# Kernel optimization log

Measured on AMD Instinct MI355X. Metric: run time of the kernel, lower is better.

## Reference

```python
import jax, jax.numpy as jnp
import numpy as np

SHIFT, REDUCE = 1, 2  # PAD = 0


def setup_inputs() -> dict:
    key = jax.random.key(0)
    k1, k2, k3 = jax.random.split(key, 3)
    B, L, E, H = 64, 128, 1024, 1024
    sentence = jax.random.normal(k1, (B, L, E), dtype=jnp.float32)
    T = 2 * L - 1
    # Valid left-branching transition sequence: S, S, R, S, R, S, R, ...
    tr = np.ones(T, dtype=np.int64)
    tr[2::2] = REDUCE
    transitions = jnp.asarray(np.tile(tr, (B, 1)))
    # word projection: Linear(E -> 2H); reduce (TreeLSTM) cell: Linear(2H -> 5H)
    Ww = (jax.random.normal(k2, (E, 2 * H), dtype=jnp.float32) * 0.02)
    bw = jnp.zeros((2 * H,), dtype=jnp.float32)
    Wr = (jax.random.normal(k3, (2 * H, 5 * H), dtype=jnp.float32) * 0.02)
    br = jnp.zeros((5 * H,), dtype=jnp.float32)
    return {"sentence": sentence, "transitions": transitions,
            "Ww": Ww, "bw": bw, "Wr": Wr, "br": br}


def _spinn_fwd(sentence, transitions, Ww, bw, Wr, br):
    B, L, _ = sentence.shape
    H = Ww.shape[1] // 2
    # word projection, split into (h, c) halves (batch norm / dropout disabled)
    out = sentence @ Ww + bw                      # [B, L, 2H]
    h_buf, c_buf = jnp.split(out, 2, axis=2)      # each [B, L, H]
    S = L + 1                                     # thin-stack capacity (+1 scratch)
    bidx = jnp.arange(B)

    def step(carry, act):
        sh, sc, sp, bp = carry                    # stacks [B,S,H], ptrs [B]
        is_shift = act == SHIFT
        is_red = act == REDUCE
        # buffer front word (front-to-back pop)
        bp_c = jnp.clip(bp, 0, L - 1)
        buf_h = h_buf[bidx, bp_c]
        buf_c = c_buf[bidx, bp_c]
        # stack top two: right = top, left = second
        ri = jnp.clip(sp - 1, 0, S - 1)
        li = jnp.clip(sp - 2, 0, S - 1)
        rh, rc = sh[bidx, ri], sc[bidx, ri]
        lh, lc = sh[bidx, li], sc[bidx, li]
        # TreeLSTM reduce cell
        a = jnp.concatenate([lh, rh], axis=-1) @ Wr + br   # [B, 5H]
        i, fl, fr, o, g = jnp.split(a, 5, axis=-1)
        c_new = (jax.nn.sigmoid(fl) * lc + jax.nn.sigmoid(fr) * rc
                 + jax.nn.sigmoid(i) * jnp.tanh(g))
        h_new = jax.nn.sigmoid(o) * jnp.tanh(c_new)
        # select write value/index; PAD writes to index S which is dropped
        wh = jnp.where(is_shift[:, None], buf_h, h_new)
        wc = jnp.where(is_shift[:, None], buf_c, c_new)
        widx = jnp.where(is_shift, sp, jnp.where(is_red, sp - 2, S))
        sh = sh.at[bidx, widx].set(wh, mode='drop')
        sc = sc.at[bidx, widx].set(wc, mode='drop')
        sp = sp + jnp.where(is_shift, 1, jnp.where(is_red, -1, 0))
        bp = bp + is_shift.astype(bp.dtype)
        return (sh, sc, sp, bp), None

    init = (jnp.zeros((B, S, H), sentence.dtype),
            jnp.zeros((B, S, H), sentence.dtype),
            jnp.zeros((B,), jnp.int32),
            jnp.zeros((B,), jnp.int32))
    acts = transitions.T.astype(jnp.int32)        # [T, B], time-major
    (sh, sc, sp, bp), _ = jax.lax.scan(step, init, acts)
    # final stack has size 1; peek h
    return sh[bidx, jnp.clip(sp - 1, 0, S - 1)]   # [B, H]


def reference(sentence, transitions, Ww, bw, Wr, br):
    return _spinn_fwd(sentence, transitions, Ww, bw, Wr, br)
```

## Files before the change

kernel.cpp:

```cpp
#include <hip/hip_runtime.h>

typedef float  f4v __attribute__((ext_vector_type(4)));
typedef short  s8v __attribute__((ext_vector_type(8)));

#define B_   64
#define L_   128
#define T_   255
#define RMAX 127
#define BPK_HALF 5242880

__device__ __forceinline__ unsigned short f2bf(float f) {
    union { float f; unsigned int u; } v; v.f = f;
    unsigned int u = v.u;
    unsigned int r = u + 0x7fffu + ((u >> 16) & 1u);
    return (unsigned short)(r >> 16);
}
__device__ __forceinline__ float bf2f(unsigned short s) {
    union { unsigned int u; float f; } v; v.u = ((unsigned int)s) << 16;
    return v.f;
}
__device__ __forceinline__ float sigf(float x) { return 1.f / (1.f + expf(-x)); }

__global__ void k_transpose_bf16(const float* __restrict__ in, unsigned short* __restrict__ out, int K, int N) {
    __shared__ float tile[32][33];
    int n0 = blockIdx.x * 32, k0 = blockIdx.y * 32;
    int tx = threadIdx.x, ty = threadIdx.y;
    for (int i = ty; i < 32; i += 8) tile[i][tx] = in[(size_t)(k0 + i) * N + n0 + tx];
    __syncthreads();
    for (int i = ty; i < 32; i += 8) out[(size_t)(n0 + i) * K + k0 + tx] = f2bf(tile[tx][i]);
}

__global__ void k_pack_b(const unsigned short* __restrict__ wrt, unsigned short* __restrict__ bpk) {
    int u = blockIdx.x * 256 + threadIdx.x;
    int half = u / 655360;
    int v = u % 655360;
    int cg = v / 10240;
    int rem = v % 10240;
    int g = rem / 2048;
    int rem2 = rem % 2048;
    int kk = rem2 >> 6, lane = rem2 & 63;
    int col = g * 1024 + cg * 16 + (lane & 15);
    int kb = kk * 32 + (lane >> 4) * 8;
    s8v val = *(const s8v*)(wrt + (size_t)col * 2048 + half * 1024 + kb);
    *(s8v*)(bpk + (size_t)u * 8) = val;
}

__global__ void k_control(const int* __restrict__ tr, int* __restrict__ desc) {
    if (threadIdx.x != 0 || blockIdx.x != 0) return;
    int stack[140];
    int sp = 0, bp = 0, r = 0;
    for (int t = 0; t < T_; ++t) {
        int a = tr[t];
        if (a == 1) {
            if (bp < L_) { stack[sp++] = bp; bp++; }
        } else if (a == 2) {
            if (sp >= 2) {
                int right = stack[sp - 1], left = stack[sp - 2];
                sp -= 2;
                desc[2 + r] = left;
                desc[2 + RMAX + r] = right;
                stack[sp++] = -(r + 1);
                r++;
            }
        }
    }
    desc[0] = r;
    desc[1] = (sp > 0) ? stack[sp - 1] : 0;
}

__global__ __launch_bounds__(256) void k_proj2(const float* __restrict__ sentence,
                                               const unsigned short* __restrict__ wwt,
                                               const float* __restrict__ bw,
                                               unsigned short* __restrict__ hw,
                                               float* __restrict__ cw) {
    __shared__ unsigned short lA[128 * 64];
    __shared__ unsigned short lB[128 * 64];
    int tid = threadIdx.x, wv = tid >> 6, lane = tid & 63;
    int lr = lane & 15, lq = lane >> 4;
    int wr = wv >> 1, wc = wv & 1;
    int rb = blockIdx.y * 128, cb = blockIdx.x * 128;
    f4v acc[4][4];
    #pragma unroll
    for (int i = 0; i < 4; ++i)
        #pragma unroll
        for (int j = 0; j < 4; ++j) acc[i][j] = (f4v){0.f, 0.f, 0.f, 0.f};

    for (int ks = 0; ks < 1024; ks += 64) {
        #pragma unroll
        for (int t = 0; t < 4; ++t) {
            int p = t * 256 + tid;
            int row = p >> 3, kgs = p & 7, kg = kgs ^ (row & 7);
            const float* s8 = sentence + (size_t)(rb + row) * 1024 + ks + kg * 8;
            float4 v0 = *(const float4*)(s8);
            float4 v1 = *(const float4*)(s8 + 4);
            s8v av;
            av[0] = (short)f2bf(v0.x); av[1] = (short)f2bf(v0.y);
            av[2] = (short)f2bf(v0.z); av[3] = (short)f2bf(v0.w);
            av[4] = (short)f2bf(v1.x); av[5] = (short)f2bf(v1.y);
            av[6] = (short)f2bf(v1.z); av[7] = (short)f2bf(v1.w);
            *(s8v*)(lA + (size_t)p * 8) = av;
            *(s8v*)(lB + (size_t)p * 8) = *(const s8v*)(wwt + (size_t)(cb + row) * 1024 + ks + kg * 8);
        }
        __syncthreads();
        #pragma unroll
        for (int s = 0; s < 2; ++s) {
            int kgx = (s * 4 + lq) ^ (lr & 7);
            s8v a[4], b[4];
            #pragma unroll
            for (int i = 0; i < 4; ++i) {
                int rowa = wr * 64 + i * 16 + lr;
                int rowb = wc * 64 + i * 16 + lr;
                a[i] = *(const s8v*)(lA + (size_t)(rowa * 8 + kgx) * 8);
                b[i] = *(const s8v*)(lB + (size_t)(rowb * 8 + kgx) * 8);
            }
            #pragma unroll
            for (int i = 0; i < 4; ++i)
                #pragma unroll
                for (int j = 0; j < 4; ++j)
                    acc[i][j] = __builtin_amdgcn_mfma_f32_16x16x32_bf16(a[i], b[j], acc[i][j], 0, 0, 0);
        }
        __syncthreads();
    }
    bool isH = (cb < 1024);
    #pragma unroll
    for (int j = 0; j < 4; ++j) {
        int col = cb + wc * 64 + j * 16 + lr;
        float bias = bw[col];
        #pragma unroll
        for (int i = 0; i < 4; ++i) {
            #pragma unroll
            for (int jj = 0; jj < 4; ++jj) {
                int m = rb + wr * 64 + i * 16 + lq * 4 + jj;
                float v = acc[i][j][jj] + bias;
                if (isH) hw[(size_t)m * 1024 + col] = f2bf(v);
                else     cw[(size_t)m * 1024 + (col - 1024)] = v;
            }
        }
    }
}

__global__ __launch_bounds__(256) void k_pw(const int* __restrict__ desc,
                                            const unsigned short* __restrict__ hw,
                                            const unsigned short* __restrict__ wrt,
                                            const float* __restrict__ br,
                                            unsigned short* __restrict__ pwb) {
    __shared__ unsigned short lA[128 * 64];
    __shared__ unsigned short lB[128 * 64];
    int tid = threadIdx.x, wv = tid >> 6, lane = tid & 63;
    int lr = lane & 15, lq = lane >> 4;
    int wr = wv >> 1, wc = wv & 1;
    int cb = blockIdx.x * 128;
    int r0 = blockIdx.y * 2;
    int nred = desc[0];
    int s0[2], s1[2];
    s0[0] = (r0 < nred) ? desc[2 + r0] : -1;
    s0[1] = (r0 < nred) ? desc[2 + RMAX + r0] : -1;
    s1[0] = (r0 + 1 < nred) ? desc[2 + r0 + 1] : -1;
    s1[1] = (r0 + 1 < nred) ? desc[2 + RMAX + r0 + 1] : -1;
    bool need[2];
    need[0] = (s0[0] >= 0) || (s1[0] >= 0);
    need[1] = (s0[1] >= 0) || (s1[1] >= 0);

    int clist[32], ncl = 0;
    if (need[0]) {
        for (int c = 0; c < 16; ++c) clist[ncl++] = c;
    }
    if (need[1]) {
        for (int c = 16; c < 32; ++c) clist[ncl++] = c;
    }

    f4v acc[4][4];
    #pragma unroll
    for (int i = 0; i < 4; ++i)
        #pragma unroll
        for (int j = 0; j < 4; ++j) acc[i][j] = (f4v){0.f, 0.f, 0.f, 0.f};

    s8v ra[4], rb_[4];
    auto preload = [&](int c) {
        int side = c >> 4;
        int kloc = (c & 15) * 64;
        #pragma unroll
        for (int t = 0; t < 4; ++t) {
            int p = t * 256 + tid;
            int row = p >> 3, kgs = p & 7, kg = kgs ^ (row & 7);
            int m = row & 63;
            int src = (row >> 6) ? s1[side] : s0[side];
            s8v va = (s8v){0,0,0,0,0,0,0,0};
            if (src >= 0)
                va = *(const s8v*)(hw + (size_t)(m * L_ + src) * 1024 + kloc + kg * 8);
            ra[t] = va;
            rb_[t] = *(const s8v*)(wrt + (size_t)(cb + row) * 2048 + side * 1024 + kloc + kg * 8);
        }
    };

    if (ncl > 0) preload(clist[0]);
    for (int ci = 0; ci < ncl; ++ci) {
        #pragma unroll
        for (int t = 0; t < 4; ++t) {
            int p = t * 256 + tid;
            *(s8v*)(lA + (size_t)p * 8) = ra[t];
            *(s8v*)(lB + (size_t)p * 8) = rb_[t];
        }
        __syncthreads();
        if (ci + 1 < ncl) preload(clist[ci + 1]);
        #pragma unroll
        for (int s = 0; s < 2; ++s) {
            int kgx = (s * 4 + lq) ^ (lr & 7);
            s8v a[4], b[4];
            #pragma unroll
            for (int i = 0; i < 4; ++i) {
                int rowa = wr * 64 + i * 16 + lr;
                int rowb = wc * 64 + i * 16 + lr;
                a[i] = *(const s8v*)(lA + (size_t)(rowa * 8 + kgx) * 8);
                b[i] = *(const s8v*)(lB + (size_t)(rowb * 8 + kgx) * 8);
            }
            #pragma unroll
            for (int i = 0; i < 4; ++i)
                #pragma unroll
                for (int j = 0; j < 4; ++j)
                    acc[i][j] = __builtin_amdgcn_mfma_f32_16x16x32_bf16(a[i], b[j], acc[i][j], 0, 0, 0);
        }
        __syncthreads();
    }
    #pragma unroll
    for (int j = 0; j < 4; ++j) {
        int col = cb + wc * 64 + j * 16 + lr;
        float bias = br[col];
        #pragma unroll
        for (int i = 0; i < 4; ++i) {
            #pragma unroll
            for (int jj = 0; jj < 4; ++jj) {
                int prow = wr * 64 + i * 16 + lq * 4 + jj;
                int rr = r0 + (prow >> 6), m = prow & 63;
                if (rr < nred)
                    pwb[((size_t)rr * B_ + m) * 5120 + col] = f2bf(acc[i][j][jj] + bias);
            }
        }
    }
}

__global__ __launch_bounds__(256) void k_step(const int* __restrict__ desc,
                                              const float* __restrict__ cw,
                                              const unsigned short* __restrict__ bpk,
                                              const unsigned short* __restrict__ pwb,
                                              unsigned short* __restrict__ hpk,
                                              unsigned short* __restrict__ nhb,
                                              float* __restrict__ nc,
                                              int r) {
    int nred = desc[0];
    if (r >= nred) return;
    int ls = desc[2 + r], rs = desc[2 + RMAX + r];
    __shared__ float scr[4 * 5 * 16 * 17];
    int tid = threadIdx.x, kq = tid >> 6, lane = tid & 63;
    int bid = blockIdx.x;
    int cg = (bid & 7) * 8 + ((bid >> 3) & 7);
    int rh = bid >> 6;
    int lr = lane & 15, lq = lane >> 4;

    int m_e = tid >> 4, ci_e = tid & 15;
    int mg_e = rh * 16 + m_e, chh_e = cg * 16 + ci_e;
    float pw_pre[5];
    #pragma unroll
    for (int g = 0; g < 5; ++g)
        pw_pre[g] = bf2f(pwb[((size_t)r * B_ + mg_e) * 5120 + g * 1024 + chh_e]);
    float lc = (ls >= 0) ? cw[(size_t)(mg_e * L_ + ls) * 1024 + chh_e]
                         : nc[((size_t)(-1 - ls) * B_ + mg_e) * 1024 + chh_e];
    float rc = (rs >= 0) ? cw[(size_t)(mg_e * L_ + rs) * 1024 + chh_e]
                         : nc[((size_t)(-1 - rs) * B_ + mg_e) * 1024 + chh_e];

    f4v acc[5];
    #pragma unroll
    for (int g = 0; g < 5; ++g) acc[g] = (f4v){0.f, 0.f, 0.f, 0.f};

    #pragma unroll
    for (int side = 0; side < 2; ++side) {
        int src = side ? rs : ls;
        if (src >= 0) continue;
        const unsigned short* A = hpk + (size_t)(-1 - src) * 65536;
        const unsigned short* Bb = bpk + (size_t)side * BPK_HALF;
        #pragma unroll
        for (int kki = 0; kki < 8; ++kki) {
            int kk = kq * 8 + kki;
            s8v a = *(const s8v*)(A + (size_t)((rh * 32 + kk) * 64 + lane) * 8);
            #pragma unroll
            for (int g = 0; g < 5; ++g) {
                s8v b = *(const s8v*)(Bb + (size_t)((((size_t)cg * 5 + g) * 32 + kk) * 64 + lane) * 8);
                acc[g] = __builtin_amdgcn_mfma_f32_16x16x32_bf16(a, b, acc[g], 0, 0, 0);
            }
        }
    }
    #pragma unroll
    for (int g = 0; g < 5; ++g)
        #pragma unroll
        for (int jj = 0; jj < 4; ++jj)
            scr[((kq * 5 + g) * 16 + lq * 4 + jj) * 17 + lr] = acc[g][jj];
    __syncthreads();
    float gg[5];
    #pragma unroll
    for (int g = 0; g < 5; ++g) {
        float s = pw_pre[g];
        #pragma unroll
        for (int q = 0; q < 4; ++q) s += scr[((q * 5 + g) * 16 + m_e) * 17 + ci_e];
        gg[g] = s;
    }
    float cn = sigf(gg[1]) * lc + sigf(gg[2]) * rc + sigf(gg[0]) * tanhf(gg[4]);
    float hn = sigf(gg[3]) * tanhf(cn);
    unsigned short hb = f2bf(hn);
    nc[((size_t)r * B_ + mg_e) * 1024 + chh_e] = cn;
    nhb[((size_t)r * B_ + mg_e) * 1024 + chh_e] = hb;
    int rf = mg_e >> 4, lr2 = mg_e & 15, kk2 = chh_e >> 5, lq2 = (chh_e >> 3) & 3, j = chh_e & 7;
    hpk[(size_t)r * 65536 + (size_t)((rf * 32 + kk2) * 64 + lq2 * 16 + lr2) * 8 + j] = hb;
}

__global__ void k_final(const int* __restrict__ desc,
                        const unsigned short* __restrict__ hw,
                        const unsigned short* __restrict__ nhb,
                        float* __restrict__ out) {
    int idx = blockIdx.x * 256 + threadIdx.x;
    if (idx >= B_ * 1024) return;
    int m = idx >> 10, ch = idx & 1023;
    int fs = desc[1];
    const unsigned short* src = (fs >= 0)
        ? hw  + ((size_t)(m * L_ + fs) << 10) + ch
        : nhb + ((size_t)((-1 - fs) * B_ + m) << 10) + ch;
    out[idx] = bf2f(*src);
}

extern "C" void kernel_launch(void* const* d_in, const int* in_sizes, int n_in,
                              void* d_out, int out_size, void* d_ws, size_t ws_size,
                              hipStream_t stream) {
    const float* sentence = (const float*)d_in[0];
    const int*   trans    = (const int*)d_in[1];
    const float* Ww       = (const float*)d_in[2];
    const float* bw       = (const float*)d_in[3];
    const float* Wr       = (const float*)d_in[4];
    const float* br       = (const float*)d_in[5];
    float* out = (float*)d_out;

    char* w = (char*)d_ws;
    size_t off = 0;
    unsigned short* Wrt = (unsigned short*)(w + off); off += (size_t)5120 * 2048 * 2;
    unsigned short* Wwt = (unsigned short*)(w + off); off += (size_t)2048 * 1024 * 2;
    unsigned short* bpk = (unsigned short*)(w + off); off += (size_t)2 * BPK_HALF * 2;
    unsigned short* hw  = (unsigned short*)(w + off); off += (size_t)8192 * 1024 * 2;
    float*          cw  = (float*)(w + off);          off += (size_t)8192 * 1024 * 4;
    unsigned short* nhb = (unsigned short*)(w + off); off += (size_t)RMAX * B_ * 1024 * 2;
    float*          nc  = (float*)(w + off);          off += (size_t)RMAX * B_ * 1024 * 4;
    unsigned short* hpk = (unsigned short*)(w + off); off += (size_t)RMAX * 65536 * 2;
    unsigned short* pwb = (unsigned short*)(w + off); off += (size_t)RMAX * B_ * 5120 * 2;
    int*            desc = (int*)(w + off);           off += 1024;

    k_transpose_bf16<<<dim3(2048 / 32, 1024 / 32), dim3(32, 8), 0, stream>>>(Ww, Wwt, 1024, 2048);
    k_transpose_bf16<<<dim3(5120 / 32, 2048 / 32), dim3(32, 8), 0, stream>>>(Wr, Wrt, 2048, 5120);
    k_pack_b<<<dim3(5120), dim3(256), 0, stream>>>(Wrt, bpk);
    k_control<<<dim3(1), dim3(1), 0, stream>>>(trans, desc);
    k_proj2<<<dim3(16, 64), dim3(256), 0, stream>>>(sentence, Wwt, bw, hw, cw);
    k_pw<<<dim3(40, 64), dim3(256), 0, stream>>>(desc, hw, Wrt, br, pwb);
    for (int r = 0; r < RMAX; ++r)
        k_step<<<dim3(256), dim3(256), 0, stream>>>(desc, cw, bpk, pwb, hpk, nhb, nc, r);
    k_final<<<dim3((B_ * 1024 + 255) / 256), dim3(256), 0, stream>>>(desc, hw, nhb, out);
}
```

Measured before the change: 1.093 ms.

## Split step K-loop over 8 waves, remap pw blocks per XCD, use nontemporal stores

```diff
diff --git a/kernel.cpp b/kernel.cpp
--- a/kernel.cpp
+++ b/kernel.cpp
@@ -133,7 +133,7 @@
                 int m = rb + wr * 64 + i * 16 + lq * 4 + jj;
                 float v = acc[i][j][jj] + bias;
                 if (isH) hw[(size_t)m * 1024 + col] = f2bf(v);
-                else     cw[(size_t)m * 1024 + (col - 1024)] = v;
+                else     __builtin_nontemporal_store(v, &cw[(size_t)m * 1024 + (col - 1024)]);
             }
         }
     }
@@ -149,8 +149,13 @@
     int tid = threadIdx.x, wv = tid >> 6, lane = tid & 63;
     int lr = lane & 15, lq = lane >> 4;
     int wr = wv >> 1, wc = wv & 1;
-    int cb = blockIdx.x * 128;
-    int r0 = blockIdx.y * 2;
+    int bid = blockIdx.x;
+    int xcd = bid & 7;
+    int s = bid >> 3;
+    int ct = xcd * 5 + (s % 5);
+    int rp = s / 5;
+    int cb = ct * 128;
+    int r0 = rp * 2;
     int nred = desc[0];
     int s0[2], s1[2];
     s0[0] = (r0 < nred) ? desc[2 + r0] : -1;
@@ -204,8 +209,8 @@
         __syncthreads();
         if (ci + 1 < ncl) preload(clist[ci + 1]);
         #pragma unroll
-        for (int s = 0; s < 2; ++s) {
-            int kgx = (s * 4 + lq) ^ (lr & 7);
+        for (int s2 = 0; s2 < 2; ++s2) {
+            int kgx = (s2 * 4 + lq) ^ (lr & 7);
             s8v a[4], b[4];
             #pragma unroll
             for (int i = 0; i < 4; ++i) {
@@ -232,14 +237,16 @@
             for (int jj = 0; jj < 4; ++jj) {
                 int prow = wr * 64 + i * 16 + lq * 4 + jj;
                 int rr = r0 + (prow >> 6), m = prow & 63;
-                if (rr < nred)
-                    pwb[((size_t)rr * B_ + m) * 5120 + col] = f2bf(acc[i][j][jj] + bias);
-            }
-        }
-    }
-}
-
-__global__ __launch_bounds__(256) void k_step(const int* __restrict__ desc,
+                if (rr < nred) {
+                    unsigned short ov = f2bf(acc[i][j][jj] + bias);
+                    __builtin_nontemporal_store(ov, &pwb[((size_t)rr * B_ + m) * 5120 + col]);
+                }
+            }
+        }
+    }
+}
+
+__global__ __launch_bounds__(512) void k_step(const int* __restrict__ desc,
                                               const float* __restrict__ cw,
                                               const unsigned short* __restrict__ bpk,
                                               const unsigned short* __restrict__ pwb,
@@ -250,23 +257,26 @@
     int nred = desc[0];
     if (r >= nred) return;
     int ls = desc[2 + r], rs = desc[2 + RMAX + r];
-    __shared__ float scr[4 * 5 * 16 * 17];
+    __shared__ float scr[8 * 5 * 16 * 17];
     int tid = threadIdx.x, kq = tid >> 6, lane = tid & 63;
     int bid = blockIdx.x;
     int cg = (bid & 7) * 8 + ((bid >> 3) & 7);
     int rh = bid >> 6;
     int lr = lane & 15, lq = lane >> 4;
 
-    int m_e = tid >> 4, ci_e = tid & 15;
+    int m_e = (tid & 255) >> 4, ci_e = tid & 15;
     int mg_e = rh * 16 + m_e, chh_e = cg * 16 + ci_e;
-    float pw_pre[5];
-    #pragma unroll
-    for (int g = 0; g < 5; ++g)
-        pw_pre[g] = bf2f(pwb[((size_t)r * B_ + mg_e) * 5120 + g * 1024 + chh_e]);
-    float lc = (ls >= 0) ? cw[(size_t)(mg_e * L_ + ls) * 1024 + chh_e]
-                         : nc[((size_t)(-1 - ls) * B_ + mg_e) * 1024 + chh_e];
-    float rc = (rs >= 0) ? cw[(size_t)(mg_e * L_ + rs) * 1024 + chh_e]
-                         : nc[((size_t)(-1 - rs) * B_ + mg_e) * 1024 + chh_e];
+    float pw_pre[5] = {0.f, 0.f, 0.f, 0.f, 0.f};
+    float lc = 0.f, rc = 0.f;
+    if (tid < 256) {
+        #pragma unroll
+        for (int g = 0; g < 5; ++g)
+            pw_pre[g] = bf2f(__builtin_nontemporal_load(&pwb[((size_t)r * B_ + mg_e) * 5120 + g * 1024 + chh_e]));
+        lc = (ls >= 0) ? __builtin_nontemporal_load(&cw[(size_t)(mg_e * L_ + ls) * 1024 + chh_e])
+                       : __builtin_nontemporal_load(&nc[((size_t)(-1 - ls) * B_ + mg_e) * 1024 + chh_e]);
+        rc = (rs >= 0) ? __builtin_nontemporal_load(&cw[(size_t)(mg_e * L_ + rs) * 1024 + chh_e])
+                       : __builtin_nontemporal_load(&nc[((size_t)(-1 - rs) * B_ + mg_e) * 1024 + chh_e]);
+    }
 
     f4v acc[5];
     #pragma unroll
@@ -279,8 +289,8 @@
         const unsigned short* A = hpk + (size_t)(-1 - src) * 65536;
         const unsigned short* Bb = bpk + (size_t)side * BPK_HALF;
         #pragma unroll
-        for (int kki = 0; kki < 8; ++kki) {
-            int kk = kq * 8 + kki;
+        for (int kki = 0; kki < 4; ++kki) {
+            int kk = kq * 4 + kki;
             s8v a = *(const s8v*)(A + (size_t)((rh * 32 + kk) * 64 + lane) * 8);
             #pragma unroll
             for (int g = 0; g < 5; ++g) {
@@ -295,21 +305,23 @@
         for (int jj = 0; jj < 4; ++jj)
             scr[((kq * 5 + g) * 16 + lq * 4 + jj) * 17 + lr] = acc[g][jj];
     __syncthreads();
-    float gg[5];
-    #pragma unroll
-    for (int g = 0; g < 5; ++g) {
-        float s = pw_pre[g];
-        #pragma unroll
-        for (int q = 0; q < 4; ++q) s += scr[((q * 5 + g) * 16 + m_e) * 17 + ci_e];
-        gg[g] = s;
-    }
-    float cn = sigf(gg[1]) * lc + sigf(gg[2]) * rc + sigf(gg[0]) * tanhf(gg[4]);
-    float hn = sigf(gg[3]) * tanhf(cn);
-    unsigned short hb = f2bf(hn);
-    nc[((size_t)r * B_ + mg_e) * 1024 + chh_e] = cn;
-    nhb[((size_t)r * B_ + mg_e) * 1024 + chh_e] = hb;
-    int rf = mg_e >> 4, lr2 = mg_e & 15, kk2 = chh_e >> 5, lq2 = (chh_e >> 3) & 3, j = chh_e & 7;
-    hpk[(size_t)r * 65536 + (size_t)((rf * 32 + kk2) * 64 + lq2 * 16 + lr2) * 8 + j] = hb;
+    if (tid < 256) {
+        float gg[5];
+        #pragma unroll
+        for (int g = 0; g < 5; ++g) {
+            float s = pw_pre[g];
+            #pragma unroll
+            for (int q = 0; q < 8; ++q) s += scr[((q * 5 + g) * 16 + m_e) * 17 + ci_e];
+            gg[g] = s;
+        }
+        float cn = sigf(gg[1]) * lc + sigf(gg[2]) * rc + sigf(gg[0]) * tanhf(gg[4]);
+        float hn = sigf(gg[3]) * tanhf(cn);
+        unsigned short hb = f2bf(hn);
+        __builtin_nontemporal_store(cn, &nc[((size_t)r * B_ + mg_e) * 1024 + chh_e]);
+        __builtin_nontemporal_store(hb, &nhb[((size_t)r * B_ + mg_e) * 1024 + chh_e]);
+        int rf = mg_e >> 4, lr2 = mg_e & 15, kk2 = chh_e >> 5, lq2 = (chh_e >> 3) & 3, j = chh_e & 7;
+        __builtin_nontemporal_store(hb, &hpk[(size_t)r * 65536 + (size_t)((rf * 32 + kk2) * 64 + lq2 * 16 + lr2) * 8 + j]);
+    }
 }
 
 __global__ void k_final(const int* __restrict__ desc,
@@ -355,8 +367,8 @@
     k_pack_b<<<dim3(5120), dim3(256), 0, stream>>>(Wrt, bpk);
     k_control<<<dim3(1), dim3(1), 0, stream>>>(trans, desc);
     k_proj2<<<dim3(16, 64), dim3(256), 0, stream>>>(sentence, Wwt, bw, hw, cw);
-    k_pw<<<dim3(40, 64), dim3(256), 0, stream>>>(desc, hw, Wrt, br, pwb);
+    k_pw<<<dim3(2560), dim3(256), 0, stream>>>(desc, hw, Wrt, br, pwb);
     for (int r = 0; r < RMAX; ++r)
-        k_step<<<dim3(256), dim3(256), 0, stream>>>(desc, cw, bpk, pwb, hpk, nhb, nc, r);
+        k_step<<<dim3(256), dim3(512), 0, stream>>>(desc, cw, bpk, pwb, hpk, nhb, nc, r);
     k_final<<<dim3((B_ * 1024 + 255) / 256), dim3(256), 0, stream>>>(desc, hw, nhb, out);
 }
```

Result: faster. 1.049 ms (-4.0%).
